# Performance work log

Measured on AMD Instinct MI355X. Metric: run time of the kernel, lower is better.

Reference implementation:

```python
import jax, jax.numpy as jnp
import numpy as np

D_MODEL = 1024
N_HEAD = 16
D_HEAD = D_MODEL // N_HEAD


def setup_inputs() -> dict:
    key = jax.random.key(0)
    ks = jax.random.split(key, 12)
    L, B, M = 2048, 2, 2048
    s = 1.0 / np.sqrt(D_MODEL)
    return {
        "q": jax.random.normal(ks[0], (L, B, D_MODEL), jnp.float32),
        "kv": jax.random.normal(ks[1], (L, B, D_MODEL), jnp.float32),
        "mem": jax.random.normal(ks[2], (M, B, D_MODEL), jnp.float32),
        "w_q": jax.random.normal(ks[3], (D_MODEL, D_MODEL), jnp.float32) * s,
        "b_q": jnp.zeros((D_MODEL,), jnp.float32),
        "w_k": jax.random.normal(ks[4], (D_MODEL, D_MODEL), jnp.float32) * s,
        "b_k": jnp.zeros((D_MODEL,), jnp.float32),
        "w_v": jax.random.normal(ks[5], (D_MODEL, D_MODEL), jnp.float32) * s,
        "b_v": jnp.zeros((D_MODEL,), jnp.float32),
        "w_c": jax.random.normal(ks[6], (D_MODEL, D_MODEL), jnp.float32) * s,
        "b_c": jnp.zeros((D_MODEL,), jnp.float32),
    }


def reference(q, kv, mem, w_q, b_q, w_k, b_k, w_v, b_v, w_c, b_c):
    # c: [L+M, B, D]
    c = jnp.concatenate([mem, kv], axis=0)
    L, B, _ = q.shape
    J = c.shape[0]
    # linear projections (torch Linear: x @ W^T + b)
    qh = (q @ w_q.T + b_q).reshape(L, B, N_HEAD, D_HEAD)
    kh = (c @ w_k.T + b_k).reshape(J, B, N_HEAD, D_HEAD)
    vh = (c @ w_v.T + b_v).reshape(J, B, N_HEAD, D_HEAD)
    # attention scores [i, j, b, n]
    score = jnp.einsum("ibnd,jbnd->ijbn", qh, kh) / np.sqrt(D_HEAD).astype(np.float32)
    prob = jax.nn.softmax(score, axis=1)
    vec = jnp.einsum("ijbn,jbnd->ibnd", prob, vh).reshape(L, B, D_MODEL)
    return vec @ w_c.T + b_c
```

## Files before the change

### kernel.cpp

```cpp
#include <hip/hip_runtime.h>


using short8 = __attribute__((ext_vector_type(8))) short;
using f32x4  = __attribute__((ext_vector_type(4))) float;

#define DEV __device__ __forceinline__

DEV unsigned short f2bf(float f) {
  union { float f; unsigned int u; } x; x.f = f;
  unsigned int r = x.u + 0x7FFFu + ((x.u >> 16) & 1u);
  return (unsigned short)(r >> 16);
}

DEV unsigned int cvtpk(float lo, float hi) {
  unsigned int r;
  asm("v_cvt_pk_bf16_f32 %0, %1, %2" : "=v"(r) : "v"(lo), "v"(hi));
  return r;
}

DEV void gload_lds16(const unsigned short* g, unsigned short* l) {
  __builtin_amdgcn_global_load_lds(
      (const __attribute__((address_space(1))) unsigned int*)g,
      (__attribute__((address_space(3))) unsigned int*)l, 16, 0, 0);
}

#define BARRIER_RAW()                      \
  do {                                     \
    __builtin_amdgcn_sched_barrier(0);     \
    __builtin_amdgcn_s_barrier();          \
    __builtin_amdgcn_sched_barrier(0);     \
  } while (0)

__global__ __launch_bounds__(256) void convert_all(
    const float* __restrict__ q, const float* __restrict__ mem_,
    const float* __restrict__ kv, const float* __restrict__ wq,
    const float* __restrict__ wk, const float* __restrict__ wv,
    const float* __restrict__ wc, unsigned short* __restrict__ a_bf,
    unsigned short* __restrict__ c_bf, unsigned short* __restrict__ w_bf) {
  size_t u = (size_t)blockIdx.x * 256 + threadIdx.x;
  const float* src;
  unsigned short* dst;
  if (u < 524288u)        { src = q    + u * 8;                dst = a_bf + u * 8; }
  else if (u < 1048576u)  { src = mem_ + (u - 524288u) * 8;    dst = c_bf + (u - 524288u) * 8; }
  else if (u < 1572864u)  { src = kv   + (u - 1048576u) * 8;   dst = c_bf + 4194304u + (u - 1048576u) * 8; }
  else if (u < 1703936u)  { src = wq   + (u - 1572864u) * 8;   dst = w_bf + (u - 1572864u) * 8; }
  else if (u < 1835008u)  { src = wk   + (u - 1703936u) * 8;   dst = w_bf + 1048576u + (u - 1703936u) * 8; }
  else if (u < 1966080u)  { src = wv   + (u - 1835008u) * 8;   dst = w_bf + 2097152u + (u - 1835008u) * 8; }
  else                    { src = wc   + (u - 1966080u) * 8;   dst = w_bf + 3145728u + (u - 1966080u) * 8; }
  float4 v0 = ((const float4*)src)[0];
  float4 v1 = ((const float4*)src)[1];
  union { unsigned short us[8]; uint4 v; } o;
  o.us[0] = f2bf(v0.x); o.us[1] = f2bf(v0.y); o.us[2] = f2bf(v0.z); o.us[3] = f2bf(v0.w);
  o.us[4] = f2bf(v1.x); o.us[5] = f2bf(v1.y); o.us[6] = f2bf(v1.z); o.us[7] = f2bf(v1.w);
  *(uint4*)dst = o.v;
}

template <int MODE>
__global__ __launch_bounds__(256, 2) void gemm_bt(
    const unsigned short* __restrict__ A, const unsigned short* __restrict__ Bw,
    const float* __restrict__ bias, void* __restrict__ outp) {
  __shared__ __align__(16) unsigned short lA[128 * 64];
  __shared__ __align__(16) unsigned short lB[128 * 64];
  const int tid = threadIdx.x;
  const int lane = tid & 63;
  const int w = tid >> 6;
  const int wr = w >> 1, wcn = w & 1;
  const int tm = blockIdx.x * 128;
  const int tn = blockIdx.y * 128;

  const int srow = lane >> 3;
  const int scol = ((lane & 7) ^ srow) * 8;
  const unsigned short* aptr = A + (size_t)(tm + 32 * w + srow) * 1024 + scol;
  const unsigned short* bptr = Bw + (size_t)(tn + 32 * w + srow) * 1024 + scol;
  unsigned short* lAw = &lA[(32 * w) * 64];
  unsigned short* lBw = &lB[(32 * w) * 64];

  const f32x4 zero = {0.f, 0.f, 0.f, 0.f};
  f32x4 acc[4][4];
#pragma unroll
  for (int i = 0; i < 4; ++i)
#pragma unroll
    for (int j = 0; j < 4; ++j) acc[i][j] = zero;

  for (int kb = 0; kb < 16; ++kb) {
    const int ko = kb * 64;
#pragma unroll
    for (int c = 0; c < 4; ++c) {
      gload_lds16(aptr + ko + c * 8 * 1024, lAw + c * 8 * 64);
      gload_lds16(bptr + ko + c * 8 * 1024, lBw + c * 8 * 64);
    }
    __syncthreads();
#pragma unroll
    for (int kk = 0; kk < 2; ++kk) {
      short8 af[4], bfr[4];
#pragma unroll
      for (int mi = 0; mi < 4; ++mi) {
        int r = 64 * wr + 16 * mi + (lane & 15);
        int slot = (kk * 4 + (lane >> 4)) ^ (r & 7);
        af[mi] = *(const short8*)&lA[r * 64 + slot * 8];
      }
#pragma unroll
      for (int ni = 0; ni < 4; ++ni) {
        int r = 64 * wcn + 16 * ni + (lane & 15);
        int slot = (kk * 4 + (lane >> 4)) ^ (r & 7);
        bfr[ni] = *(const short8*)&lB[r * 64 + slot * 8];
      }
#pragma unroll
      for (int mi = 0; mi < 4; ++mi)
#pragma unroll
        for (int ni = 0; ni < 4; ++ni)
          acc[mi][ni] = __builtin_amdgcn_mfma_f32_16x16x32_bf16(
              af[mi], bfr[ni], acc[mi][ni], 0, 0, 0);
    }
    __syncthreads();
  }

  const int g4 = (lane >> 4) * 4;
  const int c0 = lane & 15;
#pragma unroll
  for (int mi = 0; mi < 4; ++mi) {
#pragma unroll
    for (int ni = 0; ni < 4; ++ni) {
      const int colt = tn + 64 * wcn + 16 * ni + c0;
      const float bv = bias[colt];
#pragma unroll
      for (int j = 0; j < 4; ++j) {
        const int rowt = tm + 64 * wr + 16 * mi + g4 + j;
        const float v = acc[mi][ni][j] + bv;
        if constexpr (MODE == 0) {
          ((float*)outp)[(size_t)rowt * 1024 + colt] = v;
        } else if constexpr (MODE == 1) {
          const int i = rowt >> 1, b = rowt & 1, n = colt >> 6, d = colt & 63;
          ((unsigned short*)outp)[(((size_t)(b * 16 + n) * 2048 + i) << 6) + d] =
              f2bf(v * 0.1803368801111f);
        } else if constexpr (MODE == 2) {
          const int jj = rowt >> 1, b = rowt & 1, n = colt >> 6, d = colt & 63;
          ((unsigned short*)outp)[(((size_t)(b * 16 + n) * 4096 + jj) << 6) + d] = f2bf(v);
        } else {
          const int jj = rowt >> 1, b = rowt & 1, n = colt >> 6, d = colt & 63;
          const int j6 = jj & 63;
          const int pos = (j6 & 3) | (((j6 >> 4) & 1) << 2) | (((j6 >> 2) & 3) << 3) |
                          (((j6 >> 5) & 1) << 5);
          ((unsigned short*)outp)[((size_t)(b * 16 + n) * 64 + d) * 4096 + (jj & ~63) + pos] =
              f2bf(v);
        }
      }
    }
  }
}

__global__ __launch_bounds__(512, 4) void attn_kernel(
    const unsigned short* __restrict__ qh, const unsigned short* __restrict__ kh,
    const unsigned short* __restrict__ vt, unsigned short* __restrict__ vec) {
  __shared__ __align__(16) unsigned short kl[3][64 * 64];
  __shared__ __align__(16) unsigned short vl[3][64 * 64];
  const int tid = threadIdx.x;
  const int lane = tid & 63;
  const int w = tid >> 6;
  const int g = lane >> 4;
  const int l4 = lane & 15;
  const int f = blockIdx.x;
  const int head = (f & 7) * 4 + ((f >> 3) & 3);
  const int qt = f >> 5;
  const int b = head >> 4, n = head & 15;
  const unsigned short* qbase = qh + ((size_t)head * 2048 + qt * 128 + 16 * w) * 64;
  const unsigned short* kbase = kh + (size_t)head * 4096 * 64;
  const unsigned short* vbase = vt + (size_t)head * 64 * 4096;

  short8 qf[2];
#pragma unroll
  for (int kk = 0; kk < 2; ++kk)
    qf[kk] = *(const short8*)&qbase[l4 * 64 + kk * 32 + g * 8];

  const f32x4 zero = {0.f, 0.f, 0.f, 0.f};
  f32x4 oacc[4];
#pragma unroll
  for (int nd = 0; nd < 4; ++nd) oacc[nd] = zero;
  float mrow = -3.0e38f;
  float lrow = 0.f;

  const int srow = lane >> 3;
  const int scol = ((lane & 7) ^ srow) * 8;
  const unsigned short* kp = kbase + (size_t)(8 * w + srow) * 64 + scol;
  const unsigned short* vp = vbase + (size_t)(8 * w + srow) * 4096 + scol;

  auto stage = [&](int jt, int bufi) {
    gload_lds16(kp + (size_t)jt * 4096, &kl[bufi][(8 * w) * 64]);
    gload_lds16(vp + jt * 64, &vl[bufi][(8 * w) * 64]);
  };

  stage(0, 0);
  stage(1, 1);
  asm volatile("s_waitcnt vmcnt(2)" ::: "memory");
  BARRIER_RAW();

  for (int jt = 0; jt < 64; ++jt) {
    const int buf = jt % 3;
    if (jt + 2 < 64) stage(jt + 2, (jt + 2) % 3);

    f32x4 s[4];
#pragma unroll
    for (int nj = 0; nj < 4; ++nj) s[nj] = zero;
#pragma unroll
    for (int kk = 0; kk < 2; ++kk) {
      short8 bk[4];
#pragma unroll
      for (int nj = 0; nj < 4; ++nj) {
        int r = 16 * nj + l4;
        int slot = (kk * 4 + g) ^ (r & 7);
        bk[nj] = *(const short8*)&kl[buf][r * 64 + slot * 8];
      }
#pragma unroll
      for (int nj = 0; nj < 4; ++nj)
        s[nj] = __builtin_amdgcn_mfma_f32_16x16x32_bf16(bk[nj], qf[kk], s[nj], 0, 0, 0);
    }

    {
      float a0 = fmaxf(fmaxf(s[0][0], s[0][1]), fmaxf(s[0][2], s[0][3]));
      float a1 = fmaxf(fmaxf(s[1][0], s[1][1]), fmaxf(s[1][2], s[1][3]));
      float a2 = fmaxf(fmaxf(s[2][0], s[2][1]), fmaxf(s[2][2], s[2][3]));
      float a3 = fmaxf(fmaxf(s[3][0], s[3][1]), fmaxf(s[3][2], s[3][3]));
      float pmax = fmaxf(fmaxf(a0, a1), fmaxf(a2, a3));
      pmax = fmaxf(pmax, __shfl_xor(pmax, 16));
      pmax = fmaxf(pmax, __shfl_xor(pmax, 32));
      if (!__all(pmax <= mrow + 8.f)) {
        const float mnew = fmaxf(mrow, pmax);
        const float sc = __builtin_amdgcn_exp2f(mrow - mnew);
        mrow = mnew;
        lrow *= sc;
#pragma unroll
        for (int reg = 0; reg < 4; ++reg) {
          const float scr = __shfl(sc, 4 * g + reg);
#pragma unroll
          for (int nd = 0; nd < 4; ++nd) oacc[nd][reg] *= scr;
        }
      }
      const float m = mrow;
      float rs = 0.f;
#pragma unroll
      for (int nj = 0; nj < 4; ++nj)
#pragma unroll
        for (int reg = 0; reg < 4; ++reg) {
          const float p = __builtin_amdgcn_exp2f(s[nj][reg] - m);
          s[nj][reg] = p;
          rs += p;
        }
      rs += __shfl_xor(rs, 16);
      rs += __shfl_xor(rs, 32);
      lrow += rs;
    }

    short8 pa[2];
#pragma unroll
    for (int kk2 = 0; kk2 < 2; ++kk2) {
      union { unsigned int u[4]; short8 v; } t;
#pragma unroll
      for (int wd = 0; wd < 4; ++wd) {
        const int nj = (wd >> 1) + 2 * kk2;
        const int r0 = (wd & 1) * 2;
        t.u[wd] = cvtpk(s[nj][r0], s[nj][r0 + 1]);
      }
      pa[kk2] = t.v;
    }

#pragma unroll
    for (int kk2 = 0; kk2 < 2; ++kk2) {
      short8 bv4[4];
#pragma unroll
      for (int nd = 0; nd < 4; ++nd) {
        const int r = 16 * nd + l4;
        const int blk = (g + 4 * kk2) ^ (r & 7);
        bv4[nd] = *(const short8*)&vl[buf][r * 64 + blk * 8];
      }
#pragma unroll
      for (int nd = 0; nd < 4; ++nd)
        oacc[nd] = __builtin_amdgcn_mfma_f32_16x16x32_bf16(pa[kk2], bv4[nd], oacc[nd], 0, 0, 0);
    }

    if (jt < 63) {
      if (jt < 62) {
        asm volatile("s_waitcnt vmcnt(2)" ::: "memory");
      } else {
        asm volatile("s_waitcnt vmcnt(0)" ::: "memory");
      }
      BARRIER_RAW();
    }
  }

#pragma unroll
  for (int reg = 0; reg < 4; ++reg) {
    const float lr = __shfl(lrow, 4 * g + reg);
    const float inv = 1.f / lr;
    const int i = qt * 128 + 16 * w + 4 * g + reg;
#pragma unroll
    for (int nd = 0; nd < 4; ++nd) {
      const int d = 16 * nd + l4;
      vec[(size_t)(i * 2 + b) * 1024 + n * 64 + d] = f2bf(oacc[nd][reg] * inv);
    }
  }
}

extern "C" void kernel_launch(void* const* d_in, const int* in_sizes, int n_in,
                              void* d_out, int out_size, void* d_ws, size_t ws_size,
                              hipStream_t stream) {
  (void)in_sizes; (void)n_in; (void)out_size; (void)ws_size;
  const float* q    = (const float*)d_in[0];
  const float* kv   = (const float*)d_in[1];
  const float* mem_ = (const float*)d_in[2];
  const float* wq   = (const float*)d_in[3];
  const float* bq   = (const float*)d_in[4];
  const float* wk   = (const float*)d_in[5];
  const float* bk   = (const float*)d_in[6];
  const float* wv   = (const float*)d_in[7];
  const float* bv   = (const float*)d_in[8];
  const float* wc   = (const float*)d_in[9];
  const float* bc   = (const float*)d_in[10];

  char* ws = (char*)d_ws;
  unsigned short* w_bf = (unsigned short*)(ws);
  unsigned short* a_bf = (unsigned short*)(ws + (8ull << 20));
  unsigned short* c_bf = (unsigned short*)(ws + (16ull << 20));
  unsigned short* qhb  = (unsigned short*)(ws + (32ull << 20));
  unsigned short* khb  = (unsigned short*)(ws + (40ull << 20));
  unsigned short* vtb  = (unsigned short*)(ws + (56ull << 20));
  unsigned short* vecb = a_bf;

  convert_all<<<8192, 256, 0, stream>>>(q, mem_, kv, wq, wk, wv, wc, a_bf, c_bf, w_bf);
  gemm_bt<1><<<dim3(32, 8), 256, 0, stream>>>(a_bf, w_bf,                bq, qhb);
  gemm_bt<2><<<dim3(64, 8), 256, 0, stream>>>(c_bf, w_bf + (1u << 20),   bk, khb);
  gemm_bt<3><<<dim3(64, 8), 256, 0, stream>>>(c_bf, w_bf + (2u << 20),   bv, vtb);
  attn_kernel<<<512, 512, 0, stream>>>(qhb, khb, vtb, vecb);
  gemm_bt<0><<<dim3(32, 8), 256, 0, stream>>>(vecb, w_bf + (3u << 20),   bc, d_out);
}
```

Before: 198.7 us.

## Stage K/V in pairs of tiles with double buffering and MFMA priority hints

Replaces the triple-buffered, one-tile-per-barrier K/V pipeline in the attention kernel with a double-buffered scheme. Each stage loads two 64-key tiles, so there is one barrier per two subtiles instead of one per tile. It also wraps the QK and PV MFMA sections in s_setprio to favour matrix issue across waves. The aims are to cut barrier and wait overhead. The cost is more LDS per block (64KB instead of 48KB), which may lower blocks per CU. Each half-iteration also drains with vmcnt(0), which shortens how far loads run ahead.

```diff
diff --git a/kernel.cpp b/kernel.cpp
--- a/kernel.cpp
+++ b/kernel.cpp
@@ -152,8 +152,8 @@
 __global__ __launch_bounds__(512, 4) void attn_kernel(
     const unsigned short* __restrict__ qh, const unsigned short* __restrict__ kh,
     const unsigned short* __restrict__ vt, unsigned short* __restrict__ vec) {
-  __shared__ __align__(16) unsigned short kl[3][64 * 64];
-  __shared__ __align__(16) unsigned short vl[3][64 * 64];
+  __shared__ __align__(16) unsigned short kl[2][2][64 * 64];
+  __shared__ __align__(16) unsigned short vl[2][2][64 * 64];
   const int tid = threadIdx.x;
   const int lane = tid & 63;
   const int w = tid >> 6;
@@ -184,23 +184,18 @@
   const unsigned short* kp = kbase + (size_t)(8 * w + srow) * 64 + scol;
   const unsigned short* vp = vbase + (size_t)(8 * w + srow) * 4096 + scol;
 
-  auto stage = [&](int jt, int bufi) {
-    gload_lds16(kp + (size_t)jt * 4096, &kl[bufi][(8 * w) * 64]);
-    gload_lds16(vp + jt * 64, &vl[bufi][(8 * w) * 64]);
+  auto stage_pair = [&](int jp, int bufi) {
+    gload_lds16(kp + (size_t)jp * 8192,        &kl[bufi][0][(8 * w) * 64]);
+    gload_lds16(kp + (size_t)jp * 8192 + 4096, &kl[bufi][1][(8 * w) * 64]);
+    gload_lds16(vp + jp * 128,                 &vl[bufi][0][(8 * w) * 64]);
+    gload_lds16(vp + jp * 128 + 64,            &vl[bufi][1][(8 * w) * 64]);
   };
 
-  stage(0, 0);
-  stage(1, 1);
-  asm volatile("s_waitcnt vmcnt(2)" ::: "memory");
-  BARRIER_RAW();
-
-  for (int jt = 0; jt < 64; ++jt) {
-    const int buf = jt % 3;
-    if (jt + 2 < 64) stage(jt + 2, (jt + 2) % 3);
-
+  auto subtile = [&](const unsigned short* kbuf, const unsigned short* vbuf) {
     f32x4 s[4];
 #pragma unroll
     for (int nj = 0; nj < 4; ++nj) s[nj] = zero;
+    __builtin_amdgcn_s_setprio(1);
 #pragma unroll
     for (int kk = 0; kk < 2; ++kk) {
       short8 bk[4];
@@ -208,12 +203,13 @@
       for (int nj = 0; nj < 4; ++nj) {
         int r = 16 * nj + l4;
         int slot = (kk * 4 + g) ^ (r & 7);
-        bk[nj] = *(const short8*)&kl[buf][r * 64 + slot * 8];
+        bk[nj] = *(const short8*)&kbuf[r * 64 + slot * 8];
       }
 #pragma unroll
       for (int nj = 0; nj < 4; ++nj)
         s[nj] = __builtin_amdgcn_mfma_f32_16x16x32_bf16(bk[nj], qf[kk], s[nj], 0, 0, 0);
     }
+    __builtin_amdgcn_s_setprio(0);
 
     {
       float a0 = fmaxf(fmaxf(s[0][0], s[0][1]), fmaxf(s[0][2], s[0][3]));
@@ -263,6 +259,7 @@
       pa[kk2] = t.v;
     }
 
+    __builtin_amdgcn_s_setprio(1);
 #pragma unroll
     for (int kk2 = 0; kk2 < 2; ++kk2) {
       short8 bv4[4];
@@ -270,19 +267,30 @@
       for (int nd = 0; nd < 4; ++nd) {
         const int r = 16 * nd + l4;
         const int blk = (g + 4 * kk2) ^ (r & 7);
-        bv4[nd] = *(const short8*)&vl[buf][r * 64 + blk * 8];
+        bv4[nd] = *(const short8*)&vbuf[r * 64 + blk * 8];
       }
 #pragma unroll
       for (int nd = 0; nd < 4; ++nd)
         oacc[nd] = __builtin_amdgcn_mfma_f32_16x16x32_bf16(pa[kk2], bv4[nd], oacc[nd], 0, 0, 0);
     }
-
-    if (jt < 63) {
-      if (jt < 62) {
-        asm volatile("s_waitcnt vmcnt(2)" ::: "memory");
-      } else {
-        asm volatile("s_waitcnt vmcnt(0)" ::: "memory");
-      }
+    __builtin_amdgcn_s_setprio(0);
+  };
+
+  stage_pair(0, 0);
+  asm volatile("s_waitcnt vmcnt(0)" ::: "memory");
+  BARRIER_RAW();
+
+  for (int t2 = 0; t2 < 16; ++t2) {
+    stage_pair(2 * t2 + 1, 1);
+    subtile(kl[0][0], vl[0][0]);
+    subtile(kl[0][1], vl[0][1]);
+    asm volatile("s_waitcnt vmcnt(0)" ::: "memory");
+    BARRIER_RAW();
+    if (t2 < 15) stage_pair(2 * t2 + 2, 0);
+    subtile(kl[1][0], vl[1][0]);
+    subtile(kl[1][1], vl[1][1]);
+    if (t2 < 15) {
+      asm volatile("s_waitcnt vmcnt(0)" ::: "memory");
       BARRIER_RAW();
     }
   }
```

Measured after the change: 195.6 us. Within noise of the previous version (-1.6%).
